# Kernel tuning notes

Measured on AMD Instinct MI355X. Metric: run time of the kernel, lower is better.

Reference implementation:

```python
import jax, jax.numpy as jnp
import numpy as np

N_EMBD = 32
BLOCK = 8
N_HEADS = 4
HEAD = N_EMBD // N_HEADS  # 8


def setup_inputs() -> dict:
    key = jax.random.key(0)
    k_x, k_attn, k_proj, k_f1, k_f2 = jax.random.split(key, 5)
    b = 262144
    X = jax.random.normal(k_x, (b, BLOCK, N_EMBD), dtype=jnp.float32)
    # per-head fused qkv weight, stored (in, out) so y = x @ W; out = 3*HEAD, split K,Q,V
    W_attn = jax.random.normal(k_attn, (N_HEADS, N_EMBD, 3 * HEAD), dtype=jnp.float32) * 0.02
    W_proj = jax.random.normal(k_proj, (N_EMBD, N_EMBD), dtype=jnp.float32) * 0.02
    W_ff1 = jax.random.normal(k_f1, (N_EMBD, 4 * N_EMBD), dtype=jnp.float32) * 0.02
    W_ff2 = jax.random.normal(k_f2, (4 * N_EMBD, N_EMBD), dtype=jnp.float32) * 0.02
    return {"X": X, "W_attn": W_attn, "W_proj": W_proj, "W_ff1": W_ff1, "W_ff2": W_ff2}


def reference(X, W_attn, W_proj, W_ff1, W_ff2):
    b, t, c = X.shape
    # fused per-head QKV: (b, t, c) x (h, c, 3*HEAD) -> (b, h, t, 3*HEAD)
    qkv = jnp.einsum('btc,hcd->bhtd', X, W_attn)
    k, q, v = jnp.split(qkv, 3, axis=-1)  # split order K, Q, V as in torch .split
    # NOTE: scale uses full embed dim c, not head_size (faithful to source)
    scores = jnp.einsum('bhqd,bhkd->bhqk', q, k) * (c ** -0.5)
    causal = jnp.tril(jnp.ones((t, t), dtype=bool))
    scores = jnp.where(causal, scores, -jnp.inf)
    w = jax.nn.softmax(scores, axis=-1)
    attn = jnp.einsum('bhqk,bhkd->bhqd', w, v)  # (b, h, t, HEAD)
    attn = attn.transpose(0, 2, 1, 3).reshape(b, t, c)  # concat heads
    X = X + attn @ W_proj
    X = X + jax.nn.relu(X @ W_ff1) @ W_ff2
    return X
```

## Files before the change

### kernel.cpp

```cpp
#include <hip/hip_runtime.h>


typedef __attribute__((ext_vector_type(8))) short        bf16x8;
typedef __attribute__((ext_vector_type(4))) float        f32x4;
typedef __attribute__((ext_vector_type(4))) int          i32x4;
typedef __attribute__((ext_vector_type(2))) unsigned int u32x2;

#define THREADS 256
#define TPB 64
#define TPW 16

#define LDS_X     0
#define LDS_QK    1280
#define LDS_VT    3584
#define LDS_P2    5120
#define LDS_ATTN  0
#define LDS_X2    1280
#define LDS_HID   2560
#define LDS_OUT   0
#define LDS_CTX   7680

__device__ __forceinline__ unsigned pk_bf16(float a, float b) {
    unsigned r;
    asm("v_cvt_pk_bf16_f32 %0, %1, %2" : "=v"(r) : "v"(a), "v"(b));
    return r;
}

union frag_u { i32x4 i; bf16x8 b; };

__device__ __forceinline__ bf16x8 gather_w(const float* p, int ldk, int g, float s) {
    frag_u r;
    #pragma unroll
    for (int jj = 0; jj < 4; ++jj) {
        float a = p[(8 * g + 2 * jj) * ldk] * s;
        float b = p[(8 * g + 2 * jj + 1) * ldk] * s;
        r.i[jj] = (int)pk_bf16(a, b);
    }
    return r.b;
}


__device__ __forceinline__ void ph_stage(char* Wc, int lane, const f32x4& xa, const f32x4& xb) {
    i32x4 xi = { (int)pk_bf16(xa[0], xa[1]), (int)pk_bf16(xa[2], xa[3]),
                 (int)pk_bf16(xb[0], xb[1]), (int)pk_bf16(xb[2], xb[3]) };
    *(i32x4*)(void*)(Wc + LDS_X + (lane >> 2) * 80 + (lane & 3) * 16) = xi;
}

__device__ __forceinline__ void ph_qkv(char* Wc, int c, int g,
                                       const bf16x8 (&wqk)[4], const bf16x8 (&wv)[2]) {
    const f32x4 z4 = {0.f, 0.f, 0.f, 0.f};
    frag_u xf; xf.i = *(i32x4*)(void*)(Wc + LDS_X + c * 80 + g * 16);
    #pragma unroll
    for (int n = 0; n < 4; ++n) {
        f32x4 qc = __builtin_amdgcn_mfma_f32_16x16x32_bf16(wqk[n], xf.b, z4, 0, 0, 0);
        u32x2 w64 = { pk_bf16(qc[0], qc[1]), pk_bf16(qc[2], qc[3]) };
        *(u32x2*)(void*)(Wc + LDS_QK + c * 144 + (16 * n + 4 * g) * 2) = w64;
    }
    #pragma unroll
    for (int n = 0; n < 2; ++n) {
        f32x4 vc = __builtin_amdgcn_mfma_f32_16x16x32_bf16(xf.b, wv[n], z4, 0, 0, 0);
        u32x2 w64 = { pk_bf16(vc[0], vc[1]), pk_bf16(vc[2], vc[3]) };
        *(u32x2*)(void*)(Wc + LDS_VT + (16 * n + c) * 48 + 8 * g) = w64;
    }
}

__device__ __forceinline__ void ph_scores(char* Wc, int c, int g,
                                          const f32x4& mf, const i32x4& mQK) {
    const f32x4 z4 = {0.f, 0.f, 0.f, 0.f};
    #pragma unroll
    for (int h = 0; h < 4; ++h) {
        frag_u kf, qf;
        kf.i = *(i32x4*)(void*)(Wc + LDS_QK + c * 144 + 32 * h);
        qf.i = *(i32x4*)(void*)(Wc + LDS_QK + c * 144 + 32 * h + 16);
        kf.i &= mQK; qf.i &= mQK;
        f32x4 sT = __builtin_amdgcn_mfma_f32_16x16x32_bf16(kf.b, qf.b, z4, 0, 0, 0);
        float e0 = __builtin_amdgcn_exp2f(sT[0]) * mf[0];
        float e1 = __builtin_amdgcn_exp2f(sT[1]) * mf[1];
        float e2 = __builtin_amdgcn_exp2f(sT[2]) * mf[2];
        float e3 = __builtin_amdgcn_exp2f(sT[3]) * mf[3];
        float s = (e0 + e1) + (e2 + e3);
        s += __shfl_xor(s, 16);
        s += __shfl_xor(s, 32);
        float rs = __builtin_amdgcn_rcpf(s);
        u32x2 w64 = { pk_bf16(e0 * rs, e1 * rs), pk_bf16(e2 * rs, e3 * rs) };
        *(u32x2*)(void*)(Wc + LDS_P2 + (h >> 1) * 1280 + c * 80 + ((h & 1) * 16 + 4 * g) * 2) = w64;
    }
}

__device__ __forceinline__ void ph_pv(char* Wc, int c, int g, const i32x4& mPV) {
    const f32x4 z4 = {0.f, 0.f, 0.f, 0.f};
    #pragma unroll
    for (int p = 0; p < 2; ++p) {
        frag_u va, pb;
        va.i = *(i32x4*)(void*)(Wc + LDS_VT + (16 * p + c) * 48 + (g & 1) * 16);
        va.i &= mPV;
        pb.i = *(i32x4*)(void*)(Wc + LDS_P2 + p * 1280 + c * 80 + g * 16);
        f32x4 pv = __builtin_amdgcn_mfma_f32_16x16x32_bf16(va.b, pb.b, z4, 0, 0, 0);
        u32x2 w64 = { pk_bf16(pv[0], pv[1]), pk_bf16(pv[2], pv[3]) };
        *(u32x2*)(void*)(Wc + LDS_ATTN + c * 80 + (16 * p + 4 * g) * 2) = w64;
    }
}

__device__ __forceinline__ void ph_proj(char* Wc, int c, int g, const bf16x8 (&wp)[2],
                                        const f32x4& rx0, const f32x4& rx1, f32x4 (&x2c)[2]) {
    frag_u af; af.i = *(i32x4*)(void*)(Wc + LDS_ATTN + c * 80 + g * 16);
    #pragma unroll
    for (int n = 0; n < 2; ++n) {
        const f32x4 z4 = {0.f, 0.f, 0.f, 0.f};
        f32x4 pc = __builtin_amdgcn_mfma_f32_16x16x32_bf16(wp[n], af.b, z4, 0, 0, 0);
        f32x4 rx = (n == 0) ? rx0 : rx1;
        #pragma unroll
        for (int r = 0; r < 4; ++r) x2c[n][r] = pc[r] + rx[r];
        u32x2 w64 = { pk_bf16(x2c[n][0], x2c[n][1]), pk_bf16(x2c[n][2], x2c[n][3]) };
        *(u32x2*)(void*)(Wc + LDS_X2 + c * 80 + (16 * n + 4 * g) * 2) = w64;
    }
}

__device__ __forceinline__ void ph_ff1(char* Wc, int c, int g, const bf16x8 (&w1)[8]) {
    frag_u bf; bf.i = *(i32x4*)(void*)(Wc + LDS_X2 + c * 80 + g * 16);
    #pragma unroll
    for (int n = 0; n < 8; ++n) {
        const f32x4 z4 = {0.f, 0.f, 0.f, 0.f};
        f32x4 hc = __builtin_amdgcn_mfma_f32_16x16x32_bf16(w1[n], bf.b, z4, 0, 0, 0);
        #pragma unroll
        for (int r = 0; r < 4; ++r) hc[r] = fmaxf(hc[r], 0.f);
        u32x2 w64 = { pk_bf16(hc[0], hc[1]), pk_bf16(hc[2], hc[3]) };
        *(u32x2*)(void*)(Wc + LDS_HID + c * 304 + (16 * n + 4 * g) * 2) = w64;
    }
}

__device__ __forceinline__ void ph_ff2(char* Wc, int c, int g,
                                       const bf16x8 (&w2)[2][4], const f32x4 (&x2c)[2]) {
    frag_u hf0, hf1, hf2, hf3;
    hf0.i = *(i32x4*)(void*)(Wc + LDS_HID + c * 304 + 0 * 64 + g * 16);
    hf1.i = *(i32x4*)(void*)(Wc + LDS_HID + c * 304 + 1 * 64 + g * 16);
    hf2.i = *(i32x4*)(void*)(Wc + LDS_HID + c * 304 + 2 * 64 + g * 16);
    hf3.i = *(i32x4*)(void*)(Wc + LDS_HID + c * 304 + 3 * 64 + g * 16);
    #pragma unroll
    for (int n = 0; n < 2; ++n) {
        f32x4 oc = x2c[n];
        oc = __builtin_amdgcn_mfma_f32_16x16x32_bf16(w2[n][0], hf0.b, oc, 0, 0, 0);
        oc = __builtin_amdgcn_mfma_f32_16x16x32_bf16(w2[n][1], hf1.b, oc, 0, 0, 0);
        oc = __builtin_amdgcn_mfma_f32_16x16x32_bf16(w2[n][2], hf2.b, oc, 0, 0, 0);
        oc = __builtin_amdgcn_mfma_f32_16x16x32_bf16(w2[n][3], hf3.b, oc, 0, 0, 0);
        *(f32x4*)(void*)(Wc + LDS_OUT + c * 144 + (16 * n + 4 * g) * 4) = oc;
    }
}

__device__ __forceinline__ void ph_store(char* Wc, int lane, float* outg) {
    f32x4 r0 = *(f32x4*)(void*)(Wc + LDS_OUT + (lane >> 2) * 144 + (lane & 3) * 32);
    f32x4 r1 = *(f32x4*)(void*)(Wc + LDS_OUT + (lane >> 2) * 144 + (lane & 3) * 32 + 16);
    *(f32x4*)(outg + lane * 8)     = r0;
    *(f32x4*)(outg + lane * 8 + 4) = r1;
}


__global__ __launch_bounds__(THREADS)
void block_mfma(const float* __restrict__ X,
                const float* __restrict__ Wattn,
                const float* __restrict__ Wproj,
                const float* __restrict__ Wff1,
                const float* __restrict__ Wff2,
                float* __restrict__ Out,
                int ntiles)
{
    __shared__ __align__(16) char smem[4 * 2 * LDS_CTX];

    const int lane = threadIdx.x & 63;
    const int wid  = threadIdx.x >> 6;
    const int g    = lane >> 4;
    const int c    = lane & 15;
    char* WA = smem + wid * (2 * LDS_CTX);
    char* WB = WA + LDS_CTX;

    const float wscale = 0.5050098f;

    bf16x8 wqk[4], wv[2], wp[2], w1[8], w2[2][4];
    #pragma unroll
    for (int n = 0; n < 4; ++n)
        wqk[n] = gather_w(Wattn + n * 768 + c, 24, g, wscale);
    #pragma unroll
    for (int n = 0; n < 2; ++n) {
        int vch = 16 * n + c;
        wv[n] = gather_w(Wattn + (vch >> 3) * 768 + 16 + (vch & 7), 24, g, 1.f);
    }
    #pragma unroll
    for (int n = 0; n < 2; ++n)
        wp[n] = gather_w(Wproj + 16 * n + c, 32, g, 1.f);
    #pragma unroll
    for (int n = 0; n < 8; ++n)
        w1[n] = gather_w(Wff1 + 16 * n + c, 128, g, 1.f);
    #pragma unroll
    for (int n = 0; n < 2; ++n)
        #pragma unroll
        for (int ks = 0; ks < 4; ++ks)
            w2[n][ks] = gather_w(Wff2 + ks * 1024 + 16 * n + c, 32, g, 1.f);

    f32x4 mf;
    #pragma unroll
    for (int r = 0; r < 4; ++r) {
        int key = 4 * g + r;
        mf[r] = ((key >> 3) == (c >> 3) && (key & 7) <= (c & 7)) ? 1.f : 0.f;
    }
    const int b0 = (lane < 16) ? -1 : 0;
    const int b1 = (((lane >> 3) & 1) == ((lane >> 5) & 1)) ? -1 : 0;
    const i32x4 mQK = {b0, b0, b0, b0};
    const i32x4 mPV = {b1, b1, b1, b1};

    const int tile0 = blockIdx.x * TPB + wid * TPW;
    if (tile0 >= ntiles) return;

    int p0 = tile0, p1 = (tile0 + 1 < ntiles) ? tile0 + 1 : ntiles - 1;
    f32x4 xaA = *(const f32x4*)(X + (size_t)p0 * 512 + lane * 8);
    f32x4 xbA = *(const f32x4*)(X + (size_t)p0 * 512 + lane * 8 + 4);
    f32x4 xaB = *(const f32x4*)(X + (size_t)p1 * 512 + lane * 8);
    f32x4 xbB = *(const f32x4*)(X + (size_t)p1 * 512 + lane * 8 + 4);

    #pragma unroll 1
    for (int it = 0; it < TPW; it += 2) {
        const int iA = tile0 + it;
        const int iB = tile0 + it + 1;
        const int ttA = (iA < ntiles) ? iA : ntiles - 1;
        const int ttB = (iB < ntiles) ? iB : ntiles - 1;
        const float* xgA = X + (size_t)ttA * 512;
        const float* xgB = X + (size_t)ttB * 512;

        f32x4 rxA0 = *(const f32x4*)(xgA + c * 32 + 4 * g);
        f32x4 rxA1 = *(const f32x4*)(xgA + c * 32 + 16 + 4 * g);
        f32x4 rxB0 = *(const f32x4*)(xgB + c * 32 + 4 * g);
        f32x4 rxB1 = *(const f32x4*)(xgB + c * 32 + 16 + 4 * g);

        ph_stage(WA, lane, xaA, xbA);
        ph_stage(WB, lane, xaB, xbB);

        {
            int nA = (it + 2 < TPW && iA + 2 < ntiles) ? iA + 2 : ttA;
            int nB = (it + 3 < TPW && iB + 2 < ntiles) ? iB + 2 : ttB;
            xaA = *(const f32x4*)(X + (size_t)nA * 512 + lane * 8);
            xbA = *(const f32x4*)(X + (size_t)nA * 512 + lane * 8 + 4);
            xaB = *(const f32x4*)(X + (size_t)nB * 512 + lane * 8);
            xbB = *(const f32x4*)(X + (size_t)nB * 512 + lane * 8 + 4);
        }

        ph_qkv(WA, c, g, wqk, wv);
        ph_qkv(WB, c, g, wqk, wv);

        ph_scores(WA, c, g, mf, mQK);
        ph_scores(WB, c, g, mf, mQK);

        ph_pv(WA, c, g, mPV);
        ph_pv(WB, c, g, mPV);

        f32x4 x2A[2], x2B[2];
        ph_proj(WA, c, g, wp, rxA0, rxA1, x2A);
        ph_proj(WB, c, g, wp, rxB0, rxB1, x2B);

        ph_ff1(WA, c, g, w1);
        ph_ff1(WB, c, g, w1);

        ph_ff2(WA, c, g, w2, x2A);
        ph_ff2(WB, c, g, w2, x2B);

        if (iA < ntiles) ph_store(WA, lane, Out + (size_t)iA * 512);
        if (iB < ntiles) ph_store(WB, lane, Out + (size_t)iB * 512);
    }
}

extern "C" void kernel_launch(void* const* d_in, const int* in_sizes, int n_in,
                              void* d_out, int out_size, void* d_ws, size_t ws_size,
                              hipStream_t stream) {
    (void)n_in; (void)out_size; (void)d_ws; (void)ws_size;
    const float* X     = (const float*)d_in[0];
    const float* Wattn = (const float*)d_in[1];
    const float* Wproj = (const float*)d_in[2];
    const float* Wff1  = (const float*)d_in[3];
    const float* Wff2  = (const float*)d_in[4];
    float* Out = (float*)d_out;

    const int nseq   = in_sizes[0] / 256;
    const int ntiles = nseq / 2;
    const int blocks = (ntiles + TPB - 1) / TPB;
    block_mfma<<<dim3(blocks), dim3(THREADS), 0, stream>>>(
        X, Wattn, Wproj, Wff1, Wff2, Out, ntiles);
}
```

Before: 186.8 us.

## Prepack FFN weight fragments into workspace and stream them per iteration

Adds a small pre-pass kernel that converts the FF1/FF2 weights into bf16 MFMA fragments stored in the workspace. The main kernel then reloads those fragments from global memory (cache-resident) inside the loop instead of holding all 16 fragments in registers for the whole kernel. The goal is lower VGPR pressure and higher occupancy. The cost is an extra launch plus repeated cache loads each iteration. The FF1/FF2 phases are also reordered so the weight loads are spread between compute phases. A register-resident fallback path is kept for when no workspace is available.

New measurement: 198.9 us. 6.5% more time.

```diff
diff --git a/kernel.cpp b/kernel.cpp
--- a/kernel.cpp
+++ b/kernel.cpp
@@ -37,6 +37,26 @@
         r.i[jj] = (int)pk_bf16(a, b);
     }
     return r.b;
+}
+
+__global__ void pack_w(const float* __restrict__ Wff1,
+                       const float* __restrict__ Wff2,
+                       i32x4* __restrict__ ws)
+{
+    const int lane = threadIdx.x & 63;
+    const int g = lane >> 4, c = lane & 15;
+    #pragma unroll
+    for (int n = 0; n < 8; ++n) {
+        frag_u f; f.b = gather_w(Wff1 + 16 * n + c, 128, g, 1.f);
+        ws[n * 64 + lane] = f.i;
+    }
+    #pragma unroll
+    for (int n = 0; n < 2; ++n)
+        #pragma unroll
+        for (int ks = 0; ks < 4; ++ks) {
+            frag_u f; f.b = gather_w(Wff2 + ks * 1024 + 16 * n + c, 32, g, 1.f);
+            ws[(8 + n * 4 + ks) * 64 + lane] = f.i;
+        }
 }
 
 
@@ -116,12 +136,14 @@
     }
 }
 
-__device__ __forceinline__ void ph_ff1(char* Wc, int c, int g, const bf16x8 (&w1)[8]) {
-    frag_u bf; bf.i = *(i32x4*)(void*)(Wc + LDS_X2 + c * 80 + g * 16);
-    #pragma unroll
-    for (int n = 0; n < 8; ++n) {
+__device__ __forceinline__ void ph_ff1h(char* Wc, int c, int g,
+                                        const bf16x8 (&w1h)[4], int n0,
+                                        const bf16x8& bfX) {
+    #pragma unroll
+    for (int k = 0; k < 4; ++k) {
+        const int n = n0 + k;
         const f32x4 z4 = {0.f, 0.f, 0.f, 0.f};
-        f32x4 hc = __builtin_amdgcn_mfma_f32_16x16x32_bf16(w1[n], bf.b, z4, 0, 0, 0);
+        f32x4 hc = __builtin_amdgcn_mfma_f32_16x16x32_bf16(w1h[k], bfX, z4, 0, 0, 0);
         #pragma unroll
         for (int r = 0; r < 4; ++r) hc[r] = fmaxf(hc[r], 0.f);
         u32x2 w64 = { pk_bf16(hc[0], hc[1]), pk_bf16(hc[2], hc[3]) };
@@ -130,20 +152,28 @@
 }
 
 __device__ __forceinline__ void ph_ff2(char* Wc, int c, int g,
-                                       const bf16x8 (&w2)[2][4], const f32x4 (&x2c)[2]) {
+                                       const bf16x8 (&w2a)[4], const bf16x8 (&w2b)[4],
+                                       const f32x4 (&x2c)[2]) {
     frag_u hf0, hf1, hf2, hf3;
     hf0.i = *(i32x4*)(void*)(Wc + LDS_HID + c * 304 + 0 * 64 + g * 16);
     hf1.i = *(i32x4*)(void*)(Wc + LDS_HID + c * 304 + 1 * 64 + g * 16);
     hf2.i = *(i32x4*)(void*)(Wc + LDS_HID + c * 304 + 2 * 64 + g * 16);
     hf3.i = *(i32x4*)(void*)(Wc + LDS_HID + c * 304 + 3 * 64 + g * 16);
-    #pragma unroll
-    for (int n = 0; n < 2; ++n) {
-        f32x4 oc = x2c[n];
-        oc = __builtin_amdgcn_mfma_f32_16x16x32_bf16(w2[n][0], hf0.b, oc, 0, 0, 0);
-        oc = __builtin_amdgcn_mfma_f32_16x16x32_bf16(w2[n][1], hf1.b, oc, 0, 0, 0);
-        oc = __builtin_amdgcn_mfma_f32_16x16x32_bf16(w2[n][2], hf2.b, oc, 0, 0, 0);
-        oc = __builtin_amdgcn_mfma_f32_16x16x32_bf16(w2[n][3], hf3.b, oc, 0, 0, 0);
-        *(f32x4*)(void*)(Wc + LDS_OUT + c * 144 + (16 * n + 4 * g) * 4) = oc;
+    {
+        f32x4 oc = x2c[0];
+        oc = __builtin_amdgcn_mfma_f32_16x16x32_bf16(w2a[0], hf0.b, oc, 0, 0, 0);
+        oc = __builtin_amdgcn_mfma_f32_16x16x32_bf16(w2a[1], hf1.b, oc, 0, 0, 0);
+        oc = __builtin_amdgcn_mfma_f32_16x16x32_bf16(w2a[2], hf2.b, oc, 0, 0, 0);
+        oc = __builtin_amdgcn_mfma_f32_16x16x32_bf16(w2a[3], hf3.b, oc, 0, 0, 0);
+        *(f32x4*)(void*)(Wc + LDS_OUT + c * 144 + 4 * g * 4) = oc;
+    }
+    {
+        f32x4 oc = x2c[1];
+        oc = __builtin_amdgcn_mfma_f32_16x16x32_bf16(w2b[0], hf0.b, oc, 0, 0, 0);
+        oc = __builtin_amdgcn_mfma_f32_16x16x32_bf16(w2b[1], hf1.b, oc, 0, 0, 0);
+        oc = __builtin_amdgcn_mfma_f32_16x16x32_bf16(w2b[2], hf2.b, oc, 0, 0, 0);
+        oc = __builtin_amdgcn_mfma_f32_16x16x32_bf16(w2b[3], hf3.b, oc, 0, 0, 0);
+        *(f32x4*)(void*)(Wc + LDS_OUT + c * 144 + (16 + 4 * g) * 4) = oc;
     }
 }
 
@@ -155,14 +185,45 @@
 }
 
 
+struct Prolog {
+    bf16x8 wqk[4], wv[2], wp[2];
+    f32x4 mf;
+    i32x4 mQK, mPV;
+};
+
+__device__ __forceinline__ void make_prolog(Prolog& P, const float* Wattn,
+                                            const float* Wproj, int lane, int g, int c) {
+    const float wscale = 0.5050098f;
+    #pragma unroll
+    for (int n = 0; n < 4; ++n)
+        P.wqk[n] = gather_w(Wattn + n * 768 + c, 24, g, wscale);
+    #pragma unroll
+    for (int n = 0; n < 2; ++n) {
+        int vch = 16 * n + c;
+        P.wv[n] = gather_w(Wattn + (vch >> 3) * 768 + 16 + (vch & 7), 24, g, 1.f);
+    }
+    #pragma unroll
+    for (int n = 0; n < 2; ++n)
+        P.wp[n] = gather_w(Wproj + 16 * n + c, 32, g, 1.f);
+    #pragma unroll
+    for (int r = 0; r < 4; ++r) {
+        int key = 4 * g + r;
+        P.mf[r] = ((key >> 3) == (c >> 3) && (key & 7) <= (c & 7)) ? 1.f : 0.f;
+    }
+    const int b0 = (lane < 16) ? -1 : 0;
+    const int b1 = (((lane >> 3) & 1) == ((lane >> 5) & 1)) ? -1 : 0;
+    P.mQK = i32x4{b0, b0, b0, b0};
+    P.mPV = i32x4{b1, b1, b1, b1};
+}
+
+
 __global__ __launch_bounds__(THREADS)
-void block_mfma(const float* __restrict__ X,
-                const float* __restrict__ Wattn,
-                const float* __restrict__ Wproj,
-                const float* __restrict__ Wff1,
-                const float* __restrict__ Wff2,
-                float* __restrict__ Out,
-                int ntiles)
+void block_mfma_ws(const float* __restrict__ X,
+                   const float* __restrict__ Wattn,
+                   const float* __restrict__ Wproj,
+                   const i32x4* __restrict__ WT,
+                   float* __restrict__ Out,
+                   int ntiles)
 {
     __shared__ __align__(16) char smem[4 * 2 * LDS_CTX];
 
@@ -173,39 +234,8 @@
     char* WA = smem + wid * (2 * LDS_CTX);
     char* WB = WA + LDS_CTX;
 
-    const float wscale = 0.5050098f;
-
-    bf16x8 wqk[4], wv[2], wp[2], w1[8], w2[2][4];
-    #pragma unroll
-    for (int n = 0; n < 4; ++n)
-        wqk[n] = gather_w(Wattn + n * 768 + c, 24, g, wscale);
-    #pragma unroll
-    for (int n = 0; n < 2; ++n) {
-        int vch = 16 * n + c;
-        wv[n] = gather_w(Wattn + (vch >> 3) * 768 + 16 + (vch & 7), 24, g, 1.f);
-    }
-    #pragma unroll
-    for (int n = 0; n < 2; ++n)
-        wp[n] = gather_w(Wproj + 16 * n + c, 32, g, 1.f);
-    #pragma unroll
-    for (int n = 0; n < 8; ++n)
-        w1[n] = gather_w(Wff1 + 16 * n + c, 128, g, 1.f);
-    #pragma unroll
-    for (int n = 0; n < 2; ++n)
-        #pragma unroll
-        for (int ks = 0; ks < 4; ++ks)
-            w2[n][ks] = gather_w(Wff2 + ks * 1024 + 16 * n + c, 32, g, 1.f);
-
-    f32x4 mf;
-    #pragma unroll
-    for (int r = 0; r < 4; ++r) {
-        int key = 4 * g + r;
-        mf[r] = ((key >> 3) == (c >> 3) && (key & 7) <= (c & 7)) ? 1.f : 0.f;
-    }
-    const int b0 = (lane < 16) ? -1 : 0;
-    const int b1 = (((lane >> 3) & 1) == ((lane >> 5) & 1)) ? -1 : 0;
-    const i32x4 mQK = {b0, b0, b0, b0};
-    const i32x4 mPV = {b1, b1, b1, b1};
+    Prolog P;
+    make_prolog(P, Wattn, Wproj, lane, g, c);
 
     const int tile0 = blockIdx.x * TPB + wid * TPW;
     if (tile0 >= ntiles) return;
@@ -242,26 +272,143 @@
             xbB = *(const f32x4*)(X + (size_t)nB * 512 + lane * 8 + 4);
         }
 
-        ph_qkv(WA, c, g, wqk, wv);
-        ph_qkv(WB, c, g, wqk, wv);
-
-        ph_scores(WA, c, g, mf, mQK);
-        ph_scores(WB, c, g, mf, mQK);
-
-        ph_pv(WA, c, g, mPV);
-        ph_pv(WB, c, g, mPV);
+        ph_qkv(WA, c, g, P.wqk, P.wv);
+        ph_qkv(WB, c, g, P.wqk, P.wv);
+
+        bf16x8 w1lo[4];
+        #pragma unroll
+        for (int k = 0; k < 4; ++k) { frag_u t; t.i = WT[k * 64 + lane]; w1lo[k] = t.b; }
+
+        ph_scores(WA, c, g, P.mf, P.mQK);
+        ph_scores(WB, c, g, P.mf, P.mQK);
+
+        bf16x8 w1hi[4];
+        #pragma unroll
+        for (int k = 0; k < 4; ++k) { frag_u t; t.i = WT[(4 + k) * 64 + lane]; w1hi[k] = t.b; }
+
+        ph_pv(WA, c, g, P.mPV);
+        ph_pv(WB, c, g, P.mPV);
 
         f32x4 x2A[2], x2B[2];
-        ph_proj(WA, c, g, wp, rxA0, rxA1, x2A);
-        ph_proj(WB, c, g, wp, rxB0, rxB1, x2B);
-
-        ph_ff1(WA, c, g, w1);
-        ph_ff1(WB, c, g, w1);
-
-        ph_ff2(WA, c, g, w2, x2A);
-        ph_ff2(WB, c, g, w2, x2B);
-
+        ph_proj(WA, c, g, P.wp, rxA0, rxA1, x2A);
+        ph_proj(WB, c, g, P.wp, rxB0, rxB1, x2B);
+
+        frag_u bfA; bfA.i = *(i32x4*)(void*)(WA + LDS_X2 + c * 80 + g * 16);
+        frag_u bfB; bfB.i = *(i32x4*)(void*)(WB + LDS_X2 + c * 80 + g * 16);
+
+        bf16x8 w2lo[4];
+        #pragma unroll
+        for (int k = 0; k < 4; ++k) { frag_u t; t.i = WT[(8 + k) * 64 + lane]; w2lo[k] = t.b; }
+
+        ph_ff1h(WA, c, g, w1lo, 0, bfA.b);
+        ph_ff1h(WA, c, g, w1hi, 4, bfA.b);
+
+        bf16x8 w2hi[4];
+        #pragma unroll
+        for (int k = 0; k < 4; ++k) { frag_u t; t.i = WT[(12 + k) * 64 + lane]; w2hi[k] = t.b; }
+
+        ph_ff1h(WB, c, g, w1lo, 0, bfB.b);
+        ph_ff1h(WB, c, g, w1hi, 4, bfB.b);
+
+        ph_ff2(WA, c, g, w2lo, w2hi, x2A);
         if (iA < ntiles) ph_store(WA, lane, Out + (size_t)iA * 512);
+
+        ph_ff2(WB, c, g, w2lo, w2hi, x2B);
+        if (iB < ntiles) ph_store(WB, lane, Out + (size_t)iB * 512);
+    }
+}
+
+
+__global__ __launch_bounds__(THREADS)
+void block_mfma_reg(const float* __restrict__ X,
+                    const float* __restrict__ Wattn,
+                    const float* __restrict__ Wproj,
+                    const float* __restrict__ Wff1,
+                    const float* __restrict__ Wff2,
+                    float* __restrict__ Out,
+                    int ntiles)
+{
+    __shared__ __align__(16) char smem[4 * 2 * LDS_CTX];
+
+    const int lane = threadIdx.x & 63;
+    const int wid  = threadIdx.x >> 6;
+    const int g    = lane >> 4;
+    const int c    = lane & 15;
+    char* WA = smem + wid * (2 * LDS_CTX);
+    char* WB = WA + LDS_CTX;
+
+    Prolog P;
+    make_prolog(P, Wattn, Wproj, lane, g, c);
+
+    bf16x8 w1lo[4], w1hi[4], w2lo[4], w2hi[4];
+    #pragma unroll
+    for (int k = 0; k < 4; ++k) {
+        w1lo[k] = gather_w(Wff1 + 16 * k + c, 128, g, 1.f);
+        w1hi[k] = gather_w(Wff1 + 16 * (4 + k) + c, 128, g, 1.f);
+        w2lo[k] = gather_w(Wff2 + k * 1024 + c, 32, g, 1.f);
+        w2hi[k] = gather_w(Wff2 + k * 1024 + 16 + c, 32, g, 1.f);
+    }
+
+    const int tile0 = blockIdx.x * TPB + wid * TPW;
+    if (tile0 >= ntiles) return;
+
+    int p0 = tile0, p1 = (tile0 + 1 < ntiles) ? tile0 + 1 : ntiles - 1;
+    f32x4 xaA = *(const f32x4*)(X + (size_t)p0 * 512 + lane * 8);
+    f32x4 xbA = *(const f32x4*)(X + (size_t)p0 * 512 + lane * 8 + 4);
+    f32x4 xaB = *(const f32x4*)(X + (size_t)p1 * 512 + lane * 8);
+    f32x4 xbB = *(const f32x4*)(X + (size_t)p1 * 512 + lane * 8 + 4);
+
+    #pragma unroll 1
+    for (int it = 0; it < TPW; it += 2) {
+        const int iA = tile0 + it;
+        const int iB = tile0 + it + 1;
+        const int ttA = (iA < ntiles) ? iA : ntiles - 1;
+        const int ttB = (iB < ntiles) ? iB : ntiles - 1;
+        const float* xgA = X + (size_t)ttA * 512;
+        const float* xgB = X + (size_t)ttB * 512;
+
+        f32x4 rxA0 = *(const f32x4*)(xgA + c * 32 + 4 * g);
+        f32x4 rxA1 = *(const f32x4*)(xgA + c * 32 + 16 + 4 * g);
+        f32x4 rxB0 = *(const f32x4*)(xgB + c * 32 + 4 * g);
+        f32x4 rxB1 = *(const f32x4*)(xgB + c * 32 + 16 + 4 * g);
+
+        ph_stage(WA, lane, xaA, xbA);
+        ph_stage(WB, lane, xaB, xbB);
+
+        {
+            int nA = (it + 2 < TPW && iA + 2 < ntiles) ? iA + 2 : ttA;
+            int nB = (it + 3 < TPW && iB + 2 < ntiles) ? iB + 2 : ttB;
+            xaA = *(const f32x4*)(X + (size_t)nA * 512 + lane * 8);
+            xbA = *(const f32x4*)(X + (size_t)nA * 512 + lane * 8 + 4);
+            xaB = *(const f32x4*)(X + (size_t)nB * 512 + lane * 8);
+            xbB = *(const f32x4*)(X + (size_t)nB * 512 + lane * 8 + 4);
+        }
+
+        ph_qkv(WA, c, g, P.wqk, P.wv);
+        ph_qkv(WB, c, g, P.wqk, P.wv);
+
+        ph_scores(WA, c, g, P.mf, P.mQK);
+        ph_scores(WB, c, g, P.mf, P.mQK);
+
+        ph_pv(WA, c, g, P.mPV);
+        ph_pv(WB, c, g, P.mPV);
+
+        f32x4 x2A[2], x2B[2];
+        ph_proj(WA, c, g, P.wp, rxA0, rxA1, x2A);
+        ph_proj(WB, c, g, P.wp, rxB0, rxB1, x2B);
+
+        frag_u bfA; bfA.i = *(i32x4*)(void*)(WA + LDS_X2 + c * 80 + g * 16);
+        frag_u bfB; bfB.i = *(i32x4*)(void*)(WB + LDS_X2 + c * 80 + g * 16);
+
+        ph_ff1h(WA, c, g, w1lo, 0, bfA.b);
+        ph_ff1h(WA, c, g, w1hi, 4, bfA.b);
+        ph_ff1h(WB, c, g, w1lo, 0, bfB.b);
+        ph_ff1h(WB, c, g, w1hi, 4, bfB.b);
+
+        ph_ff2(WA, c, g, w2lo, w2hi, x2A);
+        if (iA < ntiles) ph_store(WA, lane, Out + (size_t)iA * 512);
+
+        ph_ff2(WB, c, g, w2lo, w2hi, x2B);
         if (iB < ntiles) ph_store(WB, lane, Out + (size_t)iB * 512);
     }
 }
@@ -269,7 +416,7 @@
 extern "C" void kernel_launch(void* const* d_in, const int* in_sizes, int n_in,
                               void* d_out, int out_size, void* d_ws, size_t ws_size,
                               hipStream_t stream) {
-    (void)n_in; (void)out_size; (void)d_ws; (void)ws_size;
+    (void)n_in; (void)out_size;
     const float* X     = (const float*)d_in[0];
     const float* Wattn = (const float*)d_in[1];
     const float* Wproj = (const float*)d_in[2];
@@ -280,6 +427,14 @@
     const int nseq   = in_sizes[0] / 256;
     const int ntiles = nseq / 2;
     const int blocks = (ntiles + TPB - 1) / TPB;
-    block_mfma<<<dim3(blocks), dim3(THREADS), 0, stream>>>(
-        X, Wattn, Wproj, Wff1, Wff2, Out, ntiles);
-}
+
+    if (ws_size >= 16384 && d_ws != nullptr) {
+        i32x4* WT = (i32x4*)d_ws;
+        pack_w<<<dim3(1), dim3(64), 0, stream>>>(Wff1, Wff2, WT);
+        block_mfma_ws<<<dim3(blocks), dim3(THREADS), 0, stream>>>(
+            X, Wattn, Wproj, WT, Out, ntiles);
+    } else {
+        block_mfma_reg<<<dim3(blocks), dim3(THREADS), 0, stream>>>(
+            X, Wattn, Wproj, Wff1, Wff2, Out, ntiles);
+    }
+}
```

## Interleave three tiles per wave and drop LDS staging of input and output

Applied to the files above, without the earlier changes.

Each wave now processes three tiles at a time instead of two, with a more compact LDS layout so three contexts fit. The bf16 X fragment is packed straight from registers loaded in MFMA order instead of being staged through LDS. The FF2 results are written directly to global memory instead of passing through an LDS output buffer. The aim is more independent MFMA work to hide latency and fewer LDS round-trips, at the cost of more register pressure, smaller blocks (48 tiles) and uncoalesced 16-byte global stores.

New measurement: 180.4 us, median of 3. 3.4% less time.

```diff
diff --git a/kernel.cpp b/kernel.cpp
--- a/kernel.cpp
+++ b/kernel.cpp
@@ -6,19 +6,21 @@
 typedef __attribute__((ext_vector_type(4))) int          i32x4;
 typedef __attribute__((ext_vector_type(2))) unsigned int u32x2;
 
+typedef i32x4 __attribute__((may_alias)) i32x4_a;
+typedef u32x2 __attribute__((may_alias)) u32x2_a;
+typedef f32x4 __attribute__((may_alias)) f32x4_a;
+
 #define THREADS 256
-#define TPB 64
-#define TPW 16
-
-#define LDS_X     0
-#define LDS_QK    1280
-#define LDS_VT    3584
-#define LDS_P2    5120
-#define LDS_ATTN  0
-#define LDS_X2    1280
-#define LDS_HID   2560
-#define LDS_OUT   0
-#define LDS_CTX   7680
+#define TPB 48
+#define TPW 12
+
+#define LDS_P2    0
+#define LDS_QK    2560
+#define LDS_ATTN  2560
+#define LDS_VT    4864
+#define LDS_X2    4864
+#define LDS_HID   0
+#define LDS_CTX   6656
 
 __device__ __forceinline__ unsigned pk_bf16(float a, float b) {
     unsigned r;
@@ -40,27 +42,21 @@
 }
 
 
-__device__ __forceinline__ void ph_stage(char* Wc, int lane, const f32x4& xa, const f32x4& xb) {
-    i32x4 xi = { (int)pk_bf16(xa[0], xa[1]), (int)pk_bf16(xa[2], xa[3]),
-                 (int)pk_bf16(xb[0], xb[1]), (int)pk_bf16(xb[2], xb[3]) };
-    *(i32x4*)(void*)(Wc + LDS_X + (lane >> 2) * 80 + (lane & 3) * 16) = xi;
-}
-
 __device__ __forceinline__ void ph_qkv(char* Wc, int c, int g,
-                                       const bf16x8 (&wqk)[4], const bf16x8 (&wv)[2]) {
+                                       const bf16x8 (&wqk)[4], const bf16x8 (&wv)[2],
+                                       const bf16x8& xf) {
     const f32x4 z4 = {0.f, 0.f, 0.f, 0.f};
-    frag_u xf; xf.i = *(i32x4*)(void*)(Wc + LDS_X + c * 80 + g * 16);
     #pragma unroll
     for (int n = 0; n < 4; ++n) {
-        f32x4 qc = __builtin_amdgcn_mfma_f32_16x16x32_bf16(wqk[n], xf.b, z4, 0, 0, 0);
+        f32x4 qc = __builtin_amdgcn_mfma_f32_16x16x32_bf16(wqk[n], xf, z4, 0, 0, 0);
         u32x2 w64 = { pk_bf16(qc[0], qc[1]), pk_bf16(qc[2], qc[3]) };
-        *(u32x2*)(void*)(Wc + LDS_QK + c * 144 + (16 * n + 4 * g) * 2) = w64;
+        *(u32x2_a*)(void*)(Wc + LDS_QK + c * 144 + (16 * n + 4 * g) * 2) = w64;
     }
     #pragma unroll
     for (int n = 0; n < 2; ++n) {
-        f32x4 vc = __builtin_amdgcn_mfma_f32_16x16x32_bf16(xf.b, wv[n], z4, 0, 0, 0);
+        f32x4 vc = __builtin_amdgcn_mfma_f32_16x16x32_bf16(xf, wv[n], z4, 0, 0, 0);
         u32x2 w64 = { pk_bf16(vc[0], vc[1]), pk_bf16(vc[2], vc[3]) };
-        *(u32x2*)(void*)(Wc + LDS_VT + (16 * n + c) * 48 + 8 * g) = w64;
+        *(u32x2_a*)(void*)(Wc + LDS_VT + (16 * n + c) * 48 + 8 * g) = w64;
     }
 }
 
@@ -70,8 +66,8 @@
     #pragma unroll
     for (int h = 0; h < 4; ++h) {
         frag_u kf, qf;
-        kf.i = *(i32x4*)(void*)(Wc + LDS_QK + c * 144 + 32 * h);
-        qf.i = *(i32x4*)(void*)(Wc + LDS_QK + c * 144 + 32 * h + 16);
+        kf.i = *(const i32x4_a*)(const void*)(Wc + LDS_QK + c * 144 + 32 * h);
+        qf.i = *(const i32x4_a*)(const void*)(Wc + LDS_QK + c * 144 + 32 * h + 16);
         kf.i &= mQK; qf.i &= mQK;
         f32x4 sT = __builtin_amdgcn_mfma_f32_16x16x32_bf16(kf.b, qf.b, z4, 0, 0, 0);
         float e0 = __builtin_amdgcn_exp2f(sT[0]) * mf[0];
@@ -83,7 +79,7 @@
         s += __shfl_xor(s, 32);
         float rs = __builtin_amdgcn_rcpf(s);
         u32x2 w64 = { pk_bf16(e0 * rs, e1 * rs), pk_bf16(e2 * rs, e3 * rs) };
-        *(u32x2*)(void*)(Wc + LDS_P2 + (h >> 1) * 1280 + c * 80 + ((h & 1) * 16 + 4 * g) * 2) = w64;
+        *(u32x2_a*)(void*)(Wc + LDS_P2 + (h >> 1) * 1280 + c * 80 + ((h & 1) * 16 + 4 * g) * 2) = w64;
     }
 }
 
@@ -92,18 +88,18 @@
     #pragma unroll
     for (int p = 0; p < 2; ++p) {
         frag_u va, pb;
-        va.i = *(i32x4*)(void*)(Wc + LDS_VT + (16 * p + c) * 48 + (g & 1) * 16);
+        va.i = *(const i32x4_a*)(const void*)(Wc + LDS_VT + (16 * p + c) * 48 + (g & 1) * 16);
         va.i &= mPV;
-        pb.i = *(i32x4*)(void*)(Wc + LDS_P2 + p * 1280 + c * 80 + g * 16);
+        pb.i = *(const i32x4_a*)(const void*)(Wc + LDS_P2 + p * 1280 + c * 80 + g * 16);
         f32x4 pv = __builtin_amdgcn_mfma_f32_16x16x32_bf16(va.b, pb.b, z4, 0, 0, 0);
         u32x2 w64 = { pk_bf16(pv[0], pv[1]), pk_bf16(pv[2], pv[3]) };
-        *(u32x2*)(void*)(Wc + LDS_ATTN + c * 80 + (16 * p + 4 * g) * 2) = w64;
+        *(u32x2_a*)(void*)(Wc + LDS_ATTN + c * 80 + (16 * p + 4 * g) * 2) = w64;
     }
 }
 
 __device__ __forceinline__ void ph_proj(char* Wc, int c, int g, const bf16x8 (&wp)[2],
                                         const f32x4& rx0, const f32x4& rx1, f32x4 (&x2c)[2]) {
-    frag_u af; af.i = *(i32x4*)(void*)(Wc + LDS_ATTN + c * 80 + g * 16);
+    frag_u af; af.i = *(const i32x4_a*)(const void*)(Wc + LDS_ATTN + c * 80 + g * 16);
     #pragma unroll
     for (int n = 0; n < 2; ++n) {
         const f32x4 z4 = {0.f, 0.f, 0.f, 0.f};
@@ -112,70 +108,74 @@
         #pragma unroll
         for (int r = 0; r < 4; ++r) x2c[n][r] = pc[r] + rx[r];
         u32x2 w64 = { pk_bf16(x2c[n][0], x2c[n][1]), pk_bf16(x2c[n][2], x2c[n][3]) };
-        *(u32x2*)(void*)(Wc + LDS_X2 + c * 80 + (16 * n + 4 * g) * 2) = w64;
-    }
-}
-
-__device__ __forceinline__ void ph_ff1(char* Wc, int c, int g, const bf16x8 (&w1)[8]) {
-    frag_u bf; bf.i = *(i32x4*)(void*)(Wc + LDS_X2 + c * 80 + g * 16);
-    #pragma unroll
-    for (int n = 0; n < 8; ++n) {
+        *(u32x2_a*)(void*)(Wc + LDS_X2 + c * 80 + (16 * n + 4 * g) * 2) = w64;
+    }
+}
+
+__device__ __forceinline__ void ph_ff1h(char* Wc, int c, int g,
+                                        const bf16x8 (&w1h)[4], int n0,
+                                        const bf16x8& bfX) {
+    #pragma unroll
+    for (int k = 0; k < 4; ++k) {
+        const int n = n0 + k;
         const f32x4 z4 = {0.f, 0.f, 0.f, 0.f};
-        f32x4 hc = __builtin_amdgcn_mfma_f32_16x16x32_bf16(w1[n], bf.b, z4, 0, 0, 0);
+        f32x4 hc = __builtin_amdgcn_mfma_f32_16x16x32_bf16(w1h[k], bfX, z4, 0, 0, 0);
         #pragma unroll
         for (int r = 0; r < 4; ++r) hc[r] = fmaxf(hc[r], 0.f);
         u32x2 w64 = { pk_bf16(hc[0], hc[1]), pk_bf16(hc[2], hc[3]) };
-        *(u32x2*)(void*)(Wc + LDS_HID + c * 304 + (16 * n + 4 * g) * 2) = w64;
-    }
-}
-
-__device__ __forceinline__ void ph_ff2(char* Wc, int c, int g,
-                                       const bf16x8 (&w2)[2][4], const f32x4 (&x2c)[2]) {
+        *(u32x2_a*)(void*)(Wc + LDS_HID + c * 272 + (16 * n + 4 * g) * 2) = w64;
+    }
+}
+
+__device__ __forceinline__ void ph_ff2_store(char* Wc, int c, int g,
+                                             const bf16x8 (&w2a)[4], const bf16x8 (&w2b)[4],
+                                             const f32x4 (&x2c)[2], float* outg, bool ok) {
     frag_u hf0, hf1, hf2, hf3;
-    hf0.i = *(i32x4*)(void*)(Wc + LDS_HID + c * 304 + 0 * 64 + g * 16);
-    hf1.i = *(i32x4*)(void*)(Wc + LDS_HID + c * 304 + 1 * 64 + g * 16);
-    hf2.i = *(i32x4*)(void*)(Wc + LDS_HID + c * 304 + 2 * 64 + g * 16);
-    hf3.i = *(i32x4*)(void*)(Wc + LDS_HID + c * 304 + 3 * 64 + g * 16);
-    #pragma unroll
-    for (int n = 0; n < 2; ++n) {
-        f32x4 oc = x2c[n];
-        oc = __builtin_amdgcn_mfma_f32_16x16x32_bf16(w2[n][0], hf0.b, oc, 0, 0, 0);
-        oc = __builtin_amdgcn_mfma_f32_16x16x32_bf16(w2[n][1], hf1.b, oc, 0, 0, 0);
-        oc = __builtin_amdgcn_mfma_f32_16x16x32_bf16(w2[n][2], hf2.b, oc, 0, 0, 0);
-        oc = __builtin_amdgcn_mfma_f32_16x16x32_bf16(w2[n][3], hf3.b, oc, 0, 0, 0);
-        *(f32x4*)(void*)(Wc + LDS_OUT + c * 144 + (16 * n + 4 * g) * 4) = oc;
-    }
-}
-
-__device__ __forceinline__ void ph_store(char* Wc, int lane, float* outg) {
-    f32x4 r0 = *(f32x4*)(void*)(Wc + LDS_OUT + (lane >> 2) * 144 + (lane & 3) * 32);
-    f32x4 r1 = *(f32x4*)(void*)(Wc + LDS_OUT + (lane >> 2) * 144 + (lane & 3) * 32 + 16);
-    *(f32x4*)(outg + lane * 8)     = r0;
-    *(f32x4*)(outg + lane * 8 + 4) = r1;
+    hf0.i = *(const i32x4_a*)(const void*)(Wc + LDS_HID + c * 272 + 0 * 64 + g * 16);
+    hf1.i = *(const i32x4_a*)(const void*)(Wc + LDS_HID + c * 272 + 1 * 64 + g * 16);
+    hf2.i = *(const i32x4_a*)(const void*)(Wc + LDS_HID + c * 272 + 2 * 64 + g * 16);
+    hf3.i = *(const i32x4_a*)(const void*)(Wc + LDS_HID + c * 272 + 3 * 64 + g * 16);
+    {
+        f32x4 oc = x2c[0];
+        oc = __builtin_amdgcn_mfma_f32_16x16x32_bf16(w2a[0], hf0.b, oc, 0, 0, 0);
+        oc = __builtin_amdgcn_mfma_f32_16x16x32_bf16(w2a[1], hf1.b, oc, 0, 0, 0);
+        oc = __builtin_amdgcn_mfma_f32_16x16x32_bf16(w2a[2], hf2.b, oc, 0, 0, 0);
+        oc = __builtin_amdgcn_mfma_f32_16x16x32_bf16(w2a[3], hf3.b, oc, 0, 0, 0);
+        if (ok) *(f32x4_a*)(outg + c * 32 + 4 * g) = oc;
+    }
+    {
+        f32x4 oc = x2c[1];
+        oc = __builtin_amdgcn_mfma_f32_16x16x32_bf16(w2b[0], hf0.b, oc, 0, 0, 0);
+        oc = __builtin_amdgcn_mfma_f32_16x16x32_bf16(w2b[1], hf1.b, oc, 0, 0, 0);
+        oc = __builtin_amdgcn_mfma_f32_16x16x32_bf16(w2b[2], hf2.b, oc, 0, 0, 0);
+        oc = __builtin_amdgcn_mfma_f32_16x16x32_bf16(w2b[3], hf3.b, oc, 0, 0, 0);
+        if (ok) *(f32x4_a*)(outg + c * 32 + 16 + 4 * g) = oc;
+    }
 }
 
 
 __global__ __launch_bounds__(THREADS)
-void block_mfma(const float* __restrict__ X,
-                const float* __restrict__ Wattn,
-                const float* __restrict__ Wproj,
-                const float* __restrict__ Wff1,
-                const float* __restrict__ Wff2,
-                float* __restrict__ Out,
-                int ntiles)
+void block_mfma3(const float* __restrict__ X,
+                 const float* __restrict__ Wattn,
+                 const float* __restrict__ Wproj,
+                 const float* __restrict__ Wff1,
+                 const float* __restrict__ Wff2,
+                 float* __restrict__ Out,
+                 int ntiles)
 {
-    __shared__ __align__(16) char smem[4 * 2 * LDS_CTX];
+    __shared__ __align__(16) char smem[4 * 3 * LDS_CTX];
 
     const int lane = threadIdx.x & 63;
     const int wid  = threadIdx.x >> 6;
     const int g    = lane >> 4;
     const int c    = lane & 15;
-    char* WA = smem + wid * (2 * LDS_CTX);
+    char* WA = smem + wid * (3 * LDS_CTX);
     char* WB = WA + LDS_CTX;
+    char* WC = WB + LDS_CTX;
 
     const float wscale = 0.5050098f;
 
-    bf16x8 wqk[4], wv[2], wp[2], w1[8], w2[2][4];
+    bf16x8 wqk[4], wv[2], wp[2], w1lo[4], w1hi[4], w2lo[4], w2hi[4];
     #pragma unroll
     for (int n = 0; n < 4; ++n)
         wqk[n] = gather_w(Wattn + n * 768 + c, 24, g, wscale);
@@ -188,13 +188,12 @@
     for (int n = 0; n < 2; ++n)
         wp[n] = gather_w(Wproj + 16 * n + c, 32, g, 1.f);
     #pragma unroll
-    for (int n = 0; n < 8; ++n)
-        w1[n] = gather_w(Wff1 + 16 * n + c, 128, g, 1.f);
-    #pragma unroll
-    for (int n = 0; n < 2; ++n)
-        #pragma unroll
-        for (int ks = 0; ks < 4; ++ks)
-            w2[n][ks] = gather_w(Wff2 + ks * 1024 + 16 * n + c, 32, g, 1.f);
+    for (int k = 0; k < 4; ++k) {
+        w1lo[k] = gather_w(Wff1 + 16 * k + c, 128, g, 1.f);
+        w1hi[k] = gather_w(Wff1 + 16 * (4 + k) + c, 128, g, 1.f);
+        w2lo[k] = gather_w(Wff2 + k * 1024 + c, 32, g, 1.f);
+        w2hi[k] = gather_w(Wff2 + k * 1024 + 16 + c, 32, g, 1.f);
+    }
 
     f32x4 mf;
     #pragma unroll
@@ -210,59 +209,86 @@
     const int tile0 = blockIdx.x * TPB + wid * TPW;
     if (tile0 >= ntiles) return;
 
-    int p0 = tile0, p1 = (tile0 + 1 < ntiles) ? tile0 + 1 : ntiles - 1;
-    f32x4 xaA = *(const f32x4*)(X + (size_t)p0 * 512 + lane * 8);
-    f32x4 xbA = *(const f32x4*)(X + (size_t)p0 * 512 + lane * 8 + 4);
-    f32x4 xaB = *(const f32x4*)(X + (size_t)p1 * 512 + lane * 8);
-    f32x4 xbB = *(const f32x4*)(X + (size_t)p1 * 512 + lane * 8 + 4);
+    int pA = tile0;
+    int pB = (tile0 + 1 < ntiles) ? tile0 + 1 : ntiles - 1;
+    int pC = (tile0 + 2 < ntiles) ? tile0 + 2 : ntiles - 1;
+    f32x4 xrA0 = *(const f32x4*)(X + (size_t)pA * 512 + c * 32 + 8 * g);
+    f32x4 xrA1 = *(const f32x4*)(X + (size_t)pA * 512 + c * 32 + 8 * g + 4);
+    f32x4 xrB0 = *(const f32x4*)(X + (size_t)pB * 512 + c * 32 + 8 * g);
+    f32x4 xrB1 = *(const f32x4*)(X + (size_t)pB * 512 + c * 32 + 8 * g + 4);
+    f32x4 xrC0 = *(const f32x4*)(X + (size_t)pC * 512 + c * 32 + 8 * g);
+    f32x4 xrC1 = *(const f32x4*)(X + (size_t)pC * 512 + c * 32 + 8 * g + 4);
 
     #pragma unroll 1
-    for (int it = 0; it < TPW; it += 2) {
+    for (int it = 0; it < TPW; it += 3) {
         const int iA = tile0 + it;
         const int iB = tile0 + it + 1;
+        const int iC = tile0 + it + 2;
         const int ttA = (iA < ntiles) ? iA : ntiles - 1;
         const int ttB = (iB < ntiles) ? iB : ntiles - 1;
+        const int ttC = (iC < ntiles) ? iC : ntiles - 1;
         const float* xgA = X + (size_t)ttA * 512;
         const float* xgB = X + (size_t)ttB * 512;
+        const float* xgC = X + (size_t)ttC * 512;
 
         f32x4 rxA0 = *(const f32x4*)(xgA + c * 32 + 4 * g);
         f32x4 rxA1 = *(const f32x4*)(xgA + c * 32 + 16 + 4 * g);
         f32x4 rxB0 = *(const f32x4*)(xgB + c * 32 + 4 * g);
         f32x4 rxB1 = *(const f32x4*)(xgB + c * 32 + 16 + 4 * g);
-
-        ph_stage(WA, lane, xaA, xbA);
-        ph_stage(WB, lane, xaB, xbB);
+        f32x4 rxC0 = *(const f32x4*)(xgC + c * 32 + 4 * g);
+        f32x4 rxC1 = *(const f32x4*)(xgC + c * 32 + 16 + 4 * g);
+
+        frag_u xfA, xfB, xfC;
+        xfA.i = i32x4{ (int)pk_bf16(xrA0[0], xrA0[1]), (int)pk_bf16(xrA0[2], xrA0[3]),
+                       (int)pk_bf16(xrA1[0], xrA1[1]), (int)pk_bf16(xrA1[2], xrA1[3]) };
+        xfB.i = i32x4{ (int)pk_bf16(xrB0[0], xrB0[1]), (int)pk_bf16(xrB0[2], xrB0[3]),
+                       (int)pk_bf16(xrB1[0], xrB1[1]), (int)pk_bf16(xrB1[2], xrB1[3]) };
+        xfC.i = i32x4{ (int)pk_bf16(xrC0[0], xrC0[1]), (int)pk_bf16(xrC0[2], xrC0[3]),
+                       (int)pk_bf16(xrC1[0], xrC1[1]), (int)pk_bf16(xrC1[2], xrC1[3]) };
 
         {
-            int nA = (it + 2 < TPW && iA + 2 < ntiles) ? iA + 2 : ttA;
-            int nB = (it + 3 < TPW && iB + 2 < ntiles) ? iB + 2 : ttB;
-            xaA = *(const f32x4*)(X + (size_t)nA * 512 + lane * 8);
-            xbA = *(const f32x4*)(X + (size_t)nA * 512 + lane * 8 + 4);
-            xaB = *(const f32x4*)(X + (size_t)nB * 512 + lane * 8);
-            xbB = *(const f32x4*)(X + (size_t)nB * 512 + lane * 8 + 4);
+            int nA = (it + 3 < TPW && iA + 3 < ntiles) ? iA + 3 : ttA;
+            int nB = (it + 4 < TPW && iB + 3 < ntiles) ? iB + 3 : ttB;
+            int nC = (it + 5 < TPW && iC + 3 < ntiles) ? iC + 3 : ttC;
+            xrA0 = *(const f32x4*)(X + (size_t)nA * 512 + c * 32 + 8 * g);
+            xrA1 = *(const f32x4*)(X + (size_t)nA * 512 + c * 32 + 8 * g + 4);
+            xrB0 = *(const f32x4*)(X + (size_t)nB * 512 + c * 32 + 8 * g);
+            xrB1 = *(const f32x4*)(X + (size_t)nB * 512 + c * 32 + 8 * g + 4);
+            xrC0 = *(const f32x4*)(X + (size_t)nC * 512 + c * 32 + 8 * g);
+            xrC1 = *(const f32x4*)(X + (size_t)nC * 512 + c * 32 + 8 * g + 4);
         }
 
-        ph_qkv(WA, c, g, wqk, wv);
-        ph_qkv(WB, c, g, wqk, wv);
+        ph_qkv(WA, c, g, wqk, wv, xfA.b);
+        ph_qkv(WB, c, g, wqk, wv, xfB.b);
+        ph_qkv(WC, c, g, wqk, wv, xfC.b);
 
         ph_scores(WA, c, g, mf, mQK);
         ph_scores(WB, c, g, mf, mQK);
+        ph_scores(WC, c, g, mf, mQK);
 
         ph_pv(WA, c, g, mPV);
         ph_pv(WB, c, g, mPV);
-
-        f32x4 x2A[2], x2B[2];
+        ph_pv(WC, c, g, mPV);
+
+        f32x4 x2A[2], x2B[2], x2C[2];
         ph_proj(WA, c, g, wp, rxA0, rxA1, x2A);
         ph_proj(WB, c, g, wp, rxB0, rxB1, x2B);
-
-        ph_ff1(WA, c, g, w1);
-        ph_ff1(WB, c, g, w1);
-
-        ph_ff2(WA, c, g, w2, x2A);
-        ph_ff2(WB, c, g, w2, x2B);
-
-        if (iA < ntiles) ph_store(WA, lane, Out + (size_t)iA * 512);
-        if (iB < ntiles) ph_store(WB, lane, Out + (size_t)iB * 512);
+        ph_proj(WC, c, g, wp, rxC0, rxC1, x2C);
+
+        frag_u bfA; bfA.i = *(const i32x4_a*)(const void*)(WA + LDS_X2 + c * 80 + g * 16);
+        frag_u bfB; bfB.i = *(const i32x4_a*)(const void*)(WB + LDS_X2 + c * 80 + g * 16);
+        frag_u bfC; bfC.i = *(const i32x4_a*)(const void*)(WC + LDS_X2 + c * 80 + g * 16);
+
+        ph_ff1h(WA, c, g, w1lo, 0, bfA.b);
+        ph_ff1h(WB, c, g, w1lo, 0, bfB.b);
+        ph_ff1h(WC, c, g, w1lo, 0, bfC.b);
+        ph_ff1h(WA, c, g, w1hi, 4, bfA.b);
+        ph_ff1h(WB, c, g, w1hi, 4, bfB.b);
+        ph_ff1h(WC, c, g, w1hi, 4, bfC.b);
+
+        ph_ff2_store(WA, c, g, w2lo, w2hi, x2A, Out + (size_t)ttA * 512, iA < ntiles);
+        ph_ff2_store(WB, c, g, w2lo, w2hi, x2B, Out + (size_t)ttB * 512, iB < ntiles);
+        ph_ff2_store(WC, c, g, w2lo, w2hi, x2C, Out + (size_t)ttC * 512, iC < ntiles);
     }
 }
 
@@ -280,6 +306,6 @@
     const int nseq   = in_sizes[0] / 256;
     const int ntiles = nseq / 2;
     const int blocks = (ntiles + TPB - 1) / TPB;
-    block_mfma<<<dim3(blocks), dim3(THREADS), 0, stream>>>(
+    block_mfma3<<<dim3(blocks), dim3(THREADS), 0, stream>>>(
         X, Wattn, Wproj, Wff1, Wff2, Out, ntiles);
 }
```
